# Optimization experiments

Hardware: AMD Instinct MI355X
Metric: run time of the kernel (lower is better)

Reference implementation:

```python
import jax, jax.numpy as jnp
import numpy as np

TEMPERATURE = 0.5

def setup_inputs() -> dict:
    key = jax.random.key(0)
    k1, k2 = jax.random.split(key)
    N, D = 4096, 256
    return {
        "z_i": jax.random.normal(k1, (N, D), dtype=jnp.float32),
        "z_j": jax.random.normal(k2, (N, D), dtype=jnp.float32),
    }

def reference(z_i, z_j):
    N = z_i.shape[0]
    z = jnp.concatenate([z_i, z_j], axis=0)                      # [2N, D]
    # cosine similarity via normalize + GEMM (same math as broadcasted CosineSimilarity)
    zn = z / jnp.linalg.norm(z, axis=-1, keepdims=True)
    sim = (zn @ zn.T) / TEMPERATURE                              # [2N, 2N]
    twoN = 2 * N
    eye = jnp.eye(twoN, dtype=bool)
    labels = jnp.arange(N, dtype=jnp.int32)
    labels = jnp.concatenate([labels, labels])
    pos_mask = (labels[None, :] == labels[:, None]) & (~eye)     # positive pairs, no diagonal
    # removing the diagonal before exp == zeroing exp on the diagonal
    exps = jnp.where(eye, 0.0, jnp.exp(sim))                     # [2N, 2N]
    pos = jnp.sum(jnp.where(pos_mask, exps, 0.0), axis=1)        # [2N]
    denom = jnp.sum(exps, axis=1)                                # [2N]
    loss = -jnp.mean(jnp.log(pos / denom))
    return loss
```

## Files before the change

### kernel.cpp

```cpp
#include <hip/hip_runtime.h>
#include <hip/hip_bf16.h>

#define TWO_N 8192
#define NHALF 4096
#define D 256
#define NTILE 64
#define BLK_ELEMS 32768
static constexpr float INV_T = 2.0f;

typedef __attribute__((ext_vector_type(8))) short short8;
typedef __attribute__((ext_vector_type(4))) float f32x4;

__device__ __forceinline__ ushort f2bfu(float f) {
    __hip_bfloat16 b = __float2bfloat16(f);
    return *reinterpret_cast<ushort*>(&b);
}

__global__ __launch_bounds__(256) void norm_pos_kernel(
        const float* __restrict__ z_i, const float* __restrict__ z_j,
        ushort* __restrict__ znb, float* __restrict__ sim_pos,
        float* __restrict__ denom) {
    const int wid = threadIdx.x >> 6, lane = threadIdx.x & 63;
    const int i = blockIdx.x * 4 + wid;
    const float4 vi = *reinterpret_cast<const float4*>(z_i + (size_t)i * D + lane * 4);
    const float4 vj = *reinterpret_cast<const float4*>(z_j + (size_t)i * D + lane * 4);
    float ssi = vi.x * vi.x + vi.y * vi.y + vi.z * vi.z + vi.w * vi.w;
    float ssj = vj.x * vj.x + vj.y * vj.y + vj.z * vj.z + vj.w * vj.w;
    float dt  = vi.x * vj.x + vi.y * vj.y + vi.z * vj.z + vi.w * vj.w;
    #pragma unroll
    for (int off = 32; off; off >>= 1) {
        ssi += __shfl_xor(ssi, off);
        ssj += __shfl_xor(ssj, off);
        dt  += __shfl_xor(dt,  off);
    }
    const float ri = rsqrtf(ssi), rj = rsqrtf(ssj);
    ushort4 oi, oj;
    oi.x = f2bfu(vi.x * ri); oi.y = f2bfu(vi.y * ri);
    oi.z = f2bfu(vi.z * ri); oi.w = f2bfu(vi.w * ri);
    oj.x = f2bfu(vj.x * rj); oj.y = f2bfu(vj.y * rj);
    oj.z = f2bfu(vj.z * rj); oj.w = f2bfu(vj.w * rj);
    const int c = lane >> 1, e = (lane & 1) * 4;
    const int i2 = i + NHALF;
    const size_t bi = ((size_t)(i  >> 7) * 32 + c) * 1024 + (i  & 127) * 8 + e;
    const size_t bj = ((size_t)(i2 >> 7) * 32 + c) * 1024 + (i2 & 127) * 8 + e;
    *reinterpret_cast<ushort4*>(znb + bi) = oi;
    *reinterpret_cast<ushort4*>(znb + bj) = oj;
    if (lane == 0) {
        const float sp = dt * ri * rj * INV_T;
        sim_pos[i] = sp;
        sim_pos[i + NHALF] = sp;
        denom[i] = 0.0f;
        denom[i + NHALF] = 0.0f;
    }
}

__global__ __launch_bounds__(256) void gemm_denom_kernel(
        const ushort* __restrict__ znb, float* __restrict__ denom) {
    const int tr = blockIdx.x;
    const int tc = blockIdx.y;
    if (tc < tr) return;

    const int tid  = threadIdx.x;
    const int lane = tid & 63;
    const int wid  = tid >> 6;
    const int wr   = wid >> 1;
    const int wc   = wid & 1;
    const int r16  = lane & 15;
    const int kgrp = lane >> 4;
    const int row0 = tr * 128;
    const int col0 = tc * 128;

    const ushort* pA = znb + (size_t)tr * BLK_ELEMS + kgrp * 1024 + (wr * 64 + r16) * 8;
    const ushort* pB = znb + (size_t)tc * BLK_ELEMS + kgrp * 1024 + (wc * 64 + r16) * 8;

    f32x4 acc[4][4];
    #pragma unroll
    for (int m = 0; m < 4; ++m)
        #pragma unroll
        for (int n = 0; n < 4; ++n) {
            f32x4 z = {0.f, 0.f, 0.f, 0.f};
            acc[m][n] = z;
        }

    #pragma unroll
    for (int ks = 0; ks < 8; ++ks) {
        short8 a[4], b[4];
        #pragma unroll
        for (int m = 0; m < 4; ++m)
            a[m] = *reinterpret_cast<const short8*>(pA + ks * 4096 + m * 128);
        #pragma unroll
        for (int n = 0; n < 4; ++n)
            b[n] = *reinterpret_cast<const short8*>(pB + ks * 4096 + n * 128);
        #pragma unroll
        for (int m = 0; m < 4; ++m)
            #pragma unroll
            for (int n = 0; n < 4; ++n)
                acc[m][n] = __builtin_amdgcn_mfma_f32_16x16x32_bf16(
                    a[m], b[n], acc[m][n], 0, 0, 0);
    }

    const bool offdiag = (tr != tc);
    float cs[4] = {0.f, 0.f, 0.f, 0.f};
    #pragma unroll
    for (int m = 0; m < 4; ++m) {
        #pragma unroll
        for (int reg = 0; reg < 4; ++reg) {
            const int rg = row0 + wr * 64 + m * 16 + kgrp * 4 + reg;
            float rs = 0.f;
            #pragma unroll
            for (int n = 0; n < 4; ++n) {
                const int cg = col0 + wc * 64 + n * 16 + r16;
                float e = __expf(acc[m][n][reg] * INV_T);
                if (rg == cg) e = 0.f;
                rs += e;
                cs[n] += e;
            }
            rs += __shfl_xor(rs, 1);
            rs += __shfl_xor(rs, 2);
            rs += __shfl_xor(rs, 4);
            rs += __shfl_xor(rs, 8);
            if (r16 == 0) atomicAdd(&denom[rg], rs);
        }
    }
    if (offdiag) {
        #pragma unroll
        for (int n = 0; n < 4; ++n) {
            cs[n] += __shfl_xor(cs[n], 16);
            cs[n] += __shfl_xor(cs[n], 32);
        }
        if (kgrp == 0) {
            #pragma unroll
            for (int n = 0; n < 4; ++n)
                atomicAdd(&denom[col0 + wc * 64 + n * 16 + r16], cs[n]);
        }
    }
}

__global__ __launch_bounds__(1024) void final_kernel(
        const float* __restrict__ sim_pos, const float* __restrict__ denom,
        float* __restrict__ out) {
    const int tid = threadIdx.x;
    float s = 0.f;
    for (int i = tid; i < TWO_N; i += 1024)
        s += sim_pos[i] - logf(denom[i]);
    #pragma unroll
    for (int off = 32; off; off >>= 1) s += __shfl_down(s, off);
    __shared__ float red[16];
    const int wid = tid >> 6, lane = tid & 63;
    if (lane == 0) red[wid] = s;
    __syncthreads();
    if (tid == 0) {
        float t = 0.f;
        #pragma unroll
        for (int w = 0; w < 16; ++w) t += red[w];
        out[0] = -t / (float)TWO_N;
    }
}

extern "C" void kernel_launch(void* const* d_in, const int* in_sizes, int n_in,
                              void* d_out, int out_size, void* d_ws, size_t ws_size,
                              hipStream_t stream) {
    const float* z_i = (const float*)d_in[0];
    const float* z_j = (const float*)d_in[1];
    float* out = (float*)d_out;

    ushort* znb     = (ushort*)d_ws;
    float*  sim_pos = (float*)((char*)d_ws + (size_t)TWO_N * D * 2);
    float*  denom   = sim_pos + TWO_N;

    norm_pos_kernel<<<NHALF / 4, 256, 0, stream>>>(z_i, z_j, znb, sim_pos, denom);
    dim3 grid(NTILE, NTILE);
    gemm_denom_kernel<<<grid, 256, 0, stream>>>(znb, denom);
    final_kernel<<<1, 1024, 0, stream>>>(sim_pos, denom, out);
}
```

Measured before the change: 58.86 us.

## Use 256x256 tiles with triple-buffered async global-to-LDS staging in GEMM

Grows the similarity GEMM tile from 128x128 to 256x256, with 512 threads (8 waves) per block. Operands are now staged through LDS using global_load_lds into a three-deep ring, with waitcnt plus barrier marking each k-step. The aim is to cut redundant global/L2 operand loads per FLOP and to overlap loads with MFMA work. The cost is 96KB of LDS per block, which probably limits occupancy to one block per CU. There are also far fewer blocks (528 upper-triangle tiles), which may leave a tail-imbalance wave across the CUs.

```diff
diff --git a/kernel.cpp b/kernel.cpp
--- a/kernel.cpp
+++ b/kernel.cpp
@@ -4,12 +4,15 @@
 #define TWO_N 8192
 #define NHALF 4096
 #define D 256
-#define NTILE 64
+#define NT256 32
 #define BLK_ELEMS 32768
 static constexpr float INV_T = 2.0f;
 
 typedef __attribute__((ext_vector_type(8))) short short8;
 typedef __attribute__((ext_vector_type(4))) float f32x4;
+
+#define AS1 __attribute__((address_space(1)))
+#define AS3 __attribute__((address_space(3)))
 
 __device__ __forceinline__ ushort f2bfu(float f) {
     __hip_bfloat16 b = __float2bfloat16(f);
@@ -54,58 +57,89 @@
     }
 }
 
-__global__ __launch_bounds__(256) void gemm_denom_kernel(
+__global__ __launch_bounds__(512, 2) void gemm_denom_kernel(
         const ushort* __restrict__ znb, float* __restrict__ denom) {
     const int tr = blockIdx.x;
     const int tc = blockIdx.y;
     if (tc < tr) return;
 
+    __shared__ ushort As[3][8192];
+    __shared__ ushort Bs[3][8192];
+
     const int tid  = threadIdx.x;
     const int lane = tid & 63;
     const int wid  = tid >> 6;
-    const int wr   = wid >> 1;
-    const int wc   = wid & 1;
+    const int wr   = wid >> 2;
+    const int wc   = wid & 3;
     const int r16  = lane & 15;
     const int kgrp = lane >> 4;
-    const int row0 = tr * 128;
-    const int col0 = tc * 128;
-
-    const ushort* pA = znb + (size_t)tr * BLK_ELEMS + kgrp * 1024 + (wr * 64 + r16) * 8;
-    const ushort* pB = znb + (size_t)tc * BLK_ELEMS + kgrp * 1024 + (wc * 64 + r16) * 8;
-
-    f32x4 acc[4][4];
-    #pragma unroll
-    for (int m = 0; m < 4; ++m)
+    const int row0 = tr * 256;
+    const int col0 = tc * 256;
+
+    const ushort* gA0 = znb + (size_t)(2 * tr) * BLK_ELEMS + tid * 8;
+    const ushort* gA1 = gA0 + BLK_ELEMS;
+    const ushort* gB0 = znb + (size_t)(2 * tc) * BLK_ELEMS + tid * 8;
+    const ushort* gB1 = gB0 + BLK_ELEMS;
+    const int dst = wid * 512;
+
+    #define STAGE(buf, koff)                                                      \
+        do {                                                                      \
+            __builtin_amdgcn_global_load_lds((const AS1 void*)(gA0 + (koff)),     \
+                (AS3 void*)(As[buf] + dst), 16, 0, 0);                            \
+            __builtin_amdgcn_global_load_lds((const AS1 void*)(gA1 + (koff)),     \
+                (AS3 void*)(As[buf] + 4096 + dst), 16, 0, 0);                     \
+            __builtin_amdgcn_global_load_lds((const AS1 void*)(gB0 + (koff)),     \
+                (AS3 void*)(Bs[buf] + dst), 16, 0, 0);                            \
+            __builtin_amdgcn_global_load_lds((const AS1 void*)(gB1 + (koff)),     \
+                (AS3 void*)(Bs[buf] + 4096 + dst), 16, 0, 0);                     \
+        } while (0)
+
+    f32x4 acc[8][4];
+    #pragma unroll
+    for (int m = 0; m < 8; ++m)
         #pragma unroll
         for (int n = 0; n < 4; ++n) {
             f32x4 z = {0.f, 0.f, 0.f, 0.f};
             acc[m][n] = z;
         }
 
+    STAGE(0, 0);
+    STAGE(1, 4096);
+
+    const int aOff = wr * 4096 + kgrp * 1024 + r16 * 8;
+    const int bOff = (wc >> 1) * 4096 + kgrp * 1024 + ((wc & 1) * 64 + r16) * 8;
+
     #pragma unroll
     for (int ks = 0; ks < 8; ++ks) {
-        short8 a[4], b[4];
-        #pragma unroll
-        for (int m = 0; m < 4; ++m)
-            a[m] = *reinterpret_cast<const short8*>(pA + ks * 4096 + m * 128);
+        const int cur = ks % 3;
+        if (ks < 7) asm volatile("s_waitcnt vmcnt(4)" ::: "memory");
+        else        asm volatile("s_waitcnt vmcnt(0)" ::: "memory");
+        __builtin_amdgcn_s_barrier();
+        asm volatile("" ::: "memory");
+        if (ks < 6) STAGE((ks + 2) % 3, (ks + 2) * 4096);
+        short8 a[8], b[4];
+        #pragma unroll
+        for (int m = 0; m < 8; ++m)
+            a[m] = *reinterpret_cast<const short8*>(As[cur] + aOff + m * 128);
         #pragma unroll
         for (int n = 0; n < 4; ++n)
-            b[n] = *reinterpret_cast<const short8*>(pB + ks * 4096 + n * 128);
-        #pragma unroll
-        for (int m = 0; m < 4; ++m)
+            b[n] = *reinterpret_cast<const short8*>(Bs[cur] + bOff + n * 128);
+        #pragma unroll
+        for (int m = 0; m < 8; ++m)
             #pragma unroll
             for (int n = 0; n < 4; ++n)
                 acc[m][n] = __builtin_amdgcn_mfma_f32_16x16x32_bf16(
                     a[m], b[n], acc[m][n], 0, 0, 0);
     }
+    #undef STAGE
 
     const bool offdiag = (tr != tc);
     float cs[4] = {0.f, 0.f, 0.f, 0.f};
     #pragma unroll
-    for (int m = 0; m < 4; ++m) {
+    for (int m = 0; m < 8; ++m) {
         #pragma unroll
         for (int reg = 0; reg < 4; ++reg) {
-            const int rg = row0 + wr * 64 + m * 16 + kgrp * 4 + reg;
+            const int rg = row0 + wr * 128 + m * 16 + kgrp * 4 + reg;
             float rs = 0.f;
             #pragma unroll
             for (int n = 0; n < 4; ++n) {
@@ -169,7 +203,7 @@
     float*  denom   = sim_pos + TWO_N;
 
     norm_pos_kernel<<<NHALF / 4, 256, 0, stream>>>(z_i, z_j, znb, sim_pos, denom);
-    dim3 grid(NTILE, NTILE);
-    gemm_denom_kernel<<<grid, 256, 0, stream>>>(znb, denom);
+    dim3 grid(NT256, NT256);
+    gemm_denom_kernel<<<grid, 512, 0, stream>>>(znb, denom);
     final_kernel<<<1, 1024, 0, stream>>>(sim_pos, denom, out);
 }
```

New measurement: 67.43 us. 1.15x slower.
